# Performance work log

Hardware: AMD Instinct MI355X
Metric: run time of the kernel (lower is better)

The kernel has to match this reference:

```python
import jax, jax.numpy as jnp
import numpy as np

B, L, LM_DIM, D, R, NUM_LAYERS, C = 32, 1024, 1024, 128, 3, 2, 8
N = B * L
E = 524288
LN_EPS = 1e-5


def setup_inputs() -> dict:
    key = jax.random.key(0)
    ks = jax.random.split(key, 16)
    inp = {
        'output': jax.random.normal(ks[0], (B, L, LM_DIM), dtype=jnp.float32),
        'edge_index': jax.random.randint(ks[1], (2, E), 0, N, dtype=jnp.int64),
        'edge_type': jax.random.randint(ks[2], (E,), 0, R, dtype=jnp.int64),
        'attention_mask': jax.random.randint(ks[3], (B, L), 0, 2, dtype=jnp.int64),
        'labels': jax.random.randint(ks[4], (B, L), 0, C, dtype=jnp.int64),
        # parameters
        'lm_W': jax.random.normal(ks[5], (D, LM_DIM), dtype=jnp.float32) * 0.02,
        'lm_b': jnp.zeros((D,), dtype=jnp.float32),
        'ln_g': jnp.ones((D,), dtype=jnp.float32),
        'ln_b': jnp.zeros((D,), dtype=jnp.float32),
        'W_rel': jax.random.normal(ks[6], (NUM_LAYERS, R, D, D), dtype=jnp.float32) * 0.05,
        'W_root': jax.random.normal(ks[7], (NUM_LAYERS, D, D), dtype=jnp.float32) * 0.05,
        'conv_b': jnp.zeros((NUM_LAYERS, D), dtype=jnp.float32),
        'cls_W': jax.random.normal(ks[8], (C, 2 * D), dtype=jnp.float32) * 0.05,
        'cls_b': jnp.zeros((C,), dtype=jnp.float32),
    }
    return inp


def _forward(output, edge_index, edge_type, attention_mask, labels,
             lm_W, lm_b, ln_g, ln_b, W_rel, W_root, conv_b, cls_W, cls_b):
    # LM head + ReLU (dropout is identity in eval) + LayerNorm
    lm = jax.nn.relu(jnp.einsum('bld,hd->blh', output, lm_W) + lm_b)
    mu = jnp.mean(lm, axis=-1, keepdims=True)
    var = jnp.mean(jnp.square(lm - mu), axis=-1, keepdims=True)
    lm = (lm - mu) * jax.lax.rsqrt(var + LN_EPS) * ln_g + ln_b  # [B,L,D]

    # RGCN over flattened nodes
    x = lm.reshape(N, D)
    src, dst = edge_index[0], edge_index[1]
    seg = dst * R + edge_type  # combined (node, relation) segment id
    ones = jnp.ones((E,), dtype=x.dtype)
    cnt = jax.ops.segment_sum(ones, seg, num_segments=N * R).reshape(N, R, 1)
    denom = jnp.maximum(cnt, 1.0)
    for layer in range(NUM_LAYERS):
        x_src = x[src]  # [E,D] gather
        sums = jax.ops.segment_sum(x_src, seg, num_segments=N * R).reshape(N, R, D)
        mean_r = sums / denom  # per-relation mean aggregation (PyG RGCNConv aggr='mean')
        out = jnp.einsum('nrd,rde->ne', mean_r, W_rel[layer])
        out = out + x @ W_root[layer] + conv_b[layer]
        x = jax.nn.relu(out)  # dropout identity

    g = x.reshape(B, L, D)
    feat = jnp.concatenate([lm, g], axis=-1)  # [B,L,2D]
    logits = jnp.einsum('blh,ch->blc', feat, cls_W) + cls_b  # [B,L,C]

    # masked cross-entropy (ignore where attention_mask != 1)
    valid = (attention_mask.reshape(-1) == 1)
    logp = jax.nn.log_softmax(logits.reshape(-1, C), axis=-1)
    nll = -jnp.take_along_axis(logp, labels.reshape(-1, 1), axis=1)[:, 0]
    n_valid = jnp.maximum(jnp.sum(valid.astype(logits.dtype)), 1.0)
    loss = jnp.sum(jnp.where(valid, nll, 0.0)) / n_valid
    return loss, logits


def reference(output, edge_index, edge_type, attention_mask, labels,
              lm_W, lm_b, ln_g, ln_b, W_rel, W_root, conv_b, cls_W, cls_b):
    return _forward(output, edge_index, edge_type, attention_mask, labels,
                    lm_W, lm_b, ln_g, ln_b, W_rel, W_root, conv_b, cls_W, cls_b)
```

## Files before the change

### kernel.cpp

```cpp
#include <hip/hip_runtime.h>

#define Bb 32
#define Ll 1024
#define LMD 1024
#define Dd 128
#define Rr 3
#define NLAYER 2
#define Cc 8
#define Nn (Bb*Ll)
#define Ee 524288
#define NSEG (Nn*Rr)
#define LN_EPS 1e-5f

typedef __attribute__((ext_vector_type(8))) short bf16x8;
typedef __attribute__((ext_vector_type(4))) float f32x4;

__device__ inline short f2bf(float f) {
    unsigned u = __builtin_bit_cast(unsigned, f);
    u += 0x7fff + ((u >> 16) & 1);
    return (short)(u >> 16);
}
__device__ inline float bf2f(unsigned short s) {
    unsigned u = ((unsigned)s) << 16;
    return __builtin_bit_cast(float, u);
}

__global__ __launch_bounds__(256) void prep_kernel(
    const float* __restrict__ lmW, const float* __restrict__ Wrel,
    const float* __restrict__ Wroot, short* __restrict__ Wp_all,
    const int* __restrict__ dst, const int* __restrict__ et,
    int* __restrict__ counts)
{
    int bid = blockIdx.x;
    if (bid < 1024) {
        int idx = bid * 256 + threadIdx.x;
        float v;
        if (idx < 131072) {
            int kk = idx & 31, n = (idx >> 5) & 127, ks = idx >> 12;
            v = lmW[n * 1024 + ks * 32 + kk];
        } else {
            int j = idx - 131072;
            int layer = j >> 16;
            int kk = j & 31, n = (j >> 5) & 127, ks = (j >> 12) & 15;
            int k = ks * 32 + kk;
            v = (k < 384) ? Wrel[(size_t)layer * 49152 + (size_t)k * 128 + n]
                          : Wroot[(size_t)layer * 16384 + (size_t)(k - 384) * 128 + n];
        }
        Wp_all[idx] = f2bf(v);
    } else {
        int e = (bid - 1024) * 256 + threadIdx.x;
        atomicAdd(&counts[dst[e] * 3 + et[e]], 1);
    }
}

__global__ __launch_bounds__(256) void lm_gemm_ln_kernel(
    const float* __restrict__ A,
    const short* __restrict__ Wp,
    const float* __restrict__ bias,
    const float* __restrict__ lng, const float* __restrict__ lnb,
    short* __restrict__ lm_bf16)
{
    const int wv   = threadIdx.x >> 6;
    const int lane = threadIdx.x & 63;
    const int m16  = lane & 15;
    const int quad = lane >> 4;
    const int row_frag = blockIdx.x * 64 + wv * 16 + m16;
    const float* arow = A + (size_t)row_frag * 1024 + quad * 8;

    f32x4 acc[8];
    #pragma unroll
    for (int i = 0; i < 8; ++i) acc[i] = (f32x4){0.f, 0.f, 0.f, 0.f};

    #pragma unroll 2
    for (int ks = 0; ks < 32; ++ks) {
        const short* wpb = Wp + ks * 4096 + m16 * 32 + quad * 8;
        bf16x8 bfr[8];
        #pragma unroll
        for (int nt = 0; nt < 8; ++nt)
            bfr[nt] = *(const bf16x8*)(wpb + nt * 512);
        const float4* ap = (const float4*)(arow + ks * 32);
        float4 a0 = ap[0], a1 = ap[1];
        union { bf16x8 v; short s[8]; } af;
        af.s[0] = f2bf(a0.x); af.s[1] = f2bf(a0.y);
        af.s[2] = f2bf(a0.z); af.s[3] = f2bf(a0.w);
        af.s[4] = f2bf(a1.x); af.s[5] = f2bf(a1.y);
        af.s[6] = f2bf(a1.z); af.s[7] = f2bf(a1.w);
        #pragma unroll
        for (int nt = 0; nt < 8; ++nt)
            acc[nt] = __builtin_amdgcn_mfma_f32_16x16x32_bf16(af.v, bfr[nt], acc[nt], 0, 0, 0);
    }

    float v[8][4];
    #pragma unroll
    for (int nt = 0; nt < 8; ++nt) {
        float bs = bias[nt * 16 + m16];
        #pragma unroll
        for (int r = 0; r < 4; ++r) v[nt][r] = fmaxf(acc[nt][r] + bs, 0.f);
    }
    float gv[8], bv[8];
    #pragma unroll
    for (int nt = 0; nt < 8; ++nt) { gv[nt] = lng[nt * 16 + m16]; bv[nt] = lnb[nt * 16 + m16]; }

    const int row0 = blockIdx.x * 64 + wv * 16 + quad * 4;
    #pragma unroll
    for (int r = 0; r < 4; ++r) {
        float s = 0.f;
        #pragma unroll
        for (int nt = 0; nt < 8; ++nt) s += v[nt][r];
        s += __shfl_xor(s, 1, 64); s += __shfl_xor(s, 2, 64);
        s += __shfl_xor(s, 4, 64); s += __shfl_xor(s, 8, 64);
        float mu = s * (1.f / 128.f);
        float q = 0.f;
        #pragma unroll
        for (int nt = 0; nt < 8; ++nt) { float d = v[nt][r] - mu; q += d * d; }
        q += __shfl_xor(q, 1, 64); q += __shfl_xor(q, 2, 64);
        q += __shfl_xor(q, 4, 64); q += __shfl_xor(q, 8, 64);
        float rs = rsqrtf(q * (1.f / 128.f) + LN_EPS);
        size_t rowoff = (size_t)(row0 + r) * 128;
        #pragma unroll
        for (int nt = 0; nt < 8; ++nt) {
            float o = (v[nt][r] - mu) * rs * gv[nt] + bv[nt];
            lm_bf16[rowoff + nt * 16 + m16] = f2bf(o);
        }
    }
}

__global__ __launch_bounds__(256) void conv_gemm_kernel(
    const short* __restrict__ A1,
    const short* __restrict__ A2,
    const short* __restrict__ Wp,
    const float* __restrict__ bias,
    short* __restrict__ out_bf16)
{
    const int wv   = threadIdx.x >> 6;
    const int lane = threadIdx.x & 63;
    const int m16  = lane & 15;
    const int quad = lane >> 4;
    const int row_frag = blockIdx.x * 64 + wv * 16 + m16;
    const short* a1row = A1 + (size_t)row_frag * 384 + quad * 8;
    const short* a2row = A2 + (size_t)row_frag * 128 + quad * 8;

    f32x4 acc[8];
    #pragma unroll
    for (int i = 0; i < 8; ++i) acc[i] = (f32x4){0.f, 0.f, 0.f, 0.f};

    #pragma unroll 2
    for (int ks = 0; ks < 16; ++ks) {
        const short* wpb = Wp + ks * 4096 + m16 * 32 + quad * 8;
        bf16x8 bfr[8];
        #pragma unroll
        for (int nt = 0; nt < 8; ++nt)
            bfr[nt] = *(const bf16x8*)(wpb + nt * 512);
        const short* ar = (ks < 12) ? (a1row + ks * 32) : (a2row + (ks - 12) * 32);
        bf16x8 af = *(const bf16x8*)ar;
        #pragma unroll
        for (int nt = 0; nt < 8; ++nt)
            acc[nt] = __builtin_amdgcn_mfma_f32_16x16x32_bf16(af, bfr[nt], acc[nt], 0, 0, 0);
    }

    const int row0 = blockIdx.x * 64 + wv * 16 + quad * 4;
    #pragma unroll
    for (int nt = 0; nt < 8; ++nt) {
        float bs = bias[nt * 16 + m16];
        #pragma unroll
        for (int r = 0; r < 4; ++r) {
            float o = fmaxf(acc[nt][r] + bs, 0.f);
            out_bf16[(size_t)(row0 + r) * 128 + nt * 16 + m16] = f2bf(o);
        }
    }
}

__global__ __launch_bounds__(256) void scan_blk_kernel(
    const int* __restrict__ counts, int* __restrict__ excl, int* __restrict__ blksum)
{
    __shared__ int wsum[4];
    int t = threadIdx.x, lane = t & 63, wv = t >> 6;
    int g = blockIdx.x * 256 + t;
    int v = counts[g];
    int x = v;
    #pragma unroll
    for (int off = 1; off < 64; off <<= 1) {
        int y = __shfl_up(x, off, 64);
        if (lane >= off) x += y;
    }
    if (lane == 63) wsum[wv] = x;
    __syncthreads();
    int woff = 0;
    for (int i = 0; i < wv; ++i) woff += wsum[i];
    excl[g] = woff + x - v;
    if (t == 255) blksum[blockIdx.x] = woff + x;
}

__global__ __launch_bounds__(256) void scan_add_kernel(
    const int* __restrict__ excl, const int* __restrict__ blksum,
    int* __restrict__ row_ptr)
{
    __shared__ int ws4[4];
    __shared__ int off_sh;
    const int t = threadIdx.x, bid = blockIdx.x;
    int s = 0;
    for (int j = t; j < bid; j += 256) s += blksum[j];
    #pragma unroll
    for (int o = 32; o > 0; o >>= 1) s += __shfl_xor(s, o, 64);
    if ((t & 63) == 0) ws4[t >> 6] = s;
    __syncthreads();
    if (t == 0) off_sh = ws4[0] + ws4[1] + ws4[2] + ws4[3];
    __syncthreads();
    int g = bid * 256 + t;
    row_ptr[g] = excl[g] + off_sh;
    if (g == 0) row_ptr[NSEG] = Ee;
}

__global__ __launch_bounds__(256) void scatter_kernel(
    const int* __restrict__ src, const int* __restrict__ dst, const int* __restrict__ et,
    const int* __restrict__ row_ptr, int* __restrict__ fill, int* __restrict__ edge_src)
{
    int e = blockIdx.x * 256 + threadIdx.x;
    int s = dst[e] * 3 + et[e];
    int pos = row_ptr[s] + atomicAdd(&fill[s], 1);
    edge_src[pos] = src[e];
}

__global__ __launch_bounds__(256) void aggregate_kernel(
    const short* __restrict__ x, const int* __restrict__ row_ptr,
    const int* __restrict__ edge_src, short* __restrict__ agg)
{
    int seg  = blockIdx.x * 4 + (threadIdx.x >> 6);
    int lane = threadIdx.x & 63;
    int b = row_ptr[seg], e = row_ptr[seg + 1];
    int n = seg / 3, r = seg - n * 3;
    float ax = 0.f, ay = 0.f;
    int i = b;
    for (; i + 4 <= e; i += 4) {
        int s0 = edge_src[i],     s1 = edge_src[i + 1];
        int s2 = edge_src[i + 2], s3 = edge_src[i + 3];
        unsigned u0 = *(const unsigned*)(x + (size_t)s0 * 128 + lane * 2);
        unsigned u1 = *(const unsigned*)(x + (size_t)s1 * 128 + lane * 2);
        unsigned u2 = *(const unsigned*)(x + (size_t)s2 * 128 + lane * 2);
        unsigned u3 = *(const unsigned*)(x + (size_t)s3 * 128 + lane * 2);
        ax += bf2f((unsigned short)(u0 & 0xffff)) + bf2f((unsigned short)(u1 & 0xffff))
            + bf2f((unsigned short)(u2 & 0xffff)) + bf2f((unsigned short)(u3 & 0xffff));
        ay += bf2f((unsigned short)(u0 >> 16)) + bf2f((unsigned short)(u1 >> 16))
            + bf2f((unsigned short)(u2 >> 16)) + bf2f((unsigned short)(u3 >> 16));
    }
    for (; i + 2 <= e; i += 2) {
        int s0 = edge_src[i], s1 = edge_src[i + 1];
        unsigned u0 = *(const unsigned*)(x + (size_t)s0 * 128 + lane * 2);
        unsigned u1 = *(const unsigned*)(x + (size_t)s1 * 128 + lane * 2);
        ax += bf2f((unsigned short)(u0 & 0xffff)) + bf2f((unsigned short)(u1 & 0xffff));
        ay += bf2f((unsigned short)(u0 >> 16))    + bf2f((unsigned short)(u1 >> 16));
    }
    if (i < e) {
        int s0 = edge_src[i];
        unsigned u0 = *(const unsigned*)(x + (size_t)s0 * 128 + lane * 2);
        ax += bf2f((unsigned short)(u0 & 0xffff));
        ay += bf2f((unsigned short)(u0 >> 16));
    }
    int cnt = e - b;
    float inv = 1.f / (float)(cnt > 0 ? cnt : 1);
    unsigned short lo = (unsigned short)f2bf(ax * inv);
    unsigned short hi = (unsigned short)f2bf(ay * inv);
    *(unsigned*)(agg + (size_t)n * 384 + r * 128 + lane * 2) = (unsigned)lo | ((unsigned)hi << 16);
}

__global__ __launch_bounds__(256) void cls_loss_kernel(
    const short* __restrict__ lm, const short* __restrict__ g,
    const float* __restrict__ clsW, const float* __restrict__ clsb,
    const int* __restrict__ mask, const int* __restrict__ labels,
    float* __restrict__ logits, float* __restrict__ accb,
    unsigned* __restrict__ ticket, float* __restrict__ loss_out)
{
    __shared__ float W[2048];
    for (int i = threadIdx.x; i < 2048; i += 256) W[i] = clsW[i];
    __syncthreads();
    int n = blockIdx.x * 256 + threadIdx.x;
    float l[8];
    #pragma unroll
    for (int c = 0; c < 8; ++c) l[c] = clsb[c];
    const short* lmr = lm + (size_t)n * 128;
    const short* gr  = g  + (size_t)n * 128;
    #pragma unroll 2
    for (int h = 0; h < 128; h += 8) {
        uint4 raw = *(const uint4*)(lmr + h);
        float a[8];
        a[0] = bf2f((unsigned short)(raw.x & 0xffff)); a[1] = bf2f((unsigned short)(raw.x >> 16));
        a[2] = bf2f((unsigned short)(raw.y & 0xffff)); a[3] = bf2f((unsigned short)(raw.y >> 16));
        a[4] = bf2f((unsigned short)(raw.z & 0xffff)); a[5] = bf2f((unsigned short)(raw.z >> 16));
        a[6] = bf2f((unsigned short)(raw.w & 0xffff)); a[7] = bf2f((unsigned short)(raw.w >> 16));
        #pragma unroll
        for (int c = 0; c < 8; ++c) {
            const float* w = &W[c * 256 + h];
            #pragma unroll
            for (int j = 0; j < 8; ++j) l[c] = fmaf(a[j], w[j], l[c]);
        }
    }
    #pragma unroll 2
    for (int h = 0; h < 128; h += 8) {
        uint4 raw = *(const uint4*)(gr + h);
        float a[8];
        a[0] = bf2f((unsigned short)(raw.x & 0xffff)); a[1] = bf2f((unsigned short)(raw.x >> 16));
        a[2] = bf2f((unsigned short)(raw.y & 0xffff)); a[3] = bf2f((unsigned short)(raw.y >> 16));
        a[4] = bf2f((unsigned short)(raw.z & 0xffff)); a[5] = bf2f((unsigned short)(raw.z >> 16));
        a[6] = bf2f((unsigned short)(raw.w & 0xffff)); a[7] = bf2f((unsigned short)(raw.w >> 16));
        #pragma unroll
        for (int c = 0; c < 8; ++c) {
            const float* w = &W[c * 256 + 128 + h];
            #pragma unroll
            for (int j = 0; j < 8; ++j) l[c] = fmaf(a[j], w[j], l[c]);
        }
    }
    #pragma unroll
    for (int c = 0; c < 8; ++c) logits[(size_t)n * 8 + c] = l[c];

    float m = l[0];
    #pragma unroll
    for (int c = 1; c < 8; ++c) m = fmaxf(m, l[c]);
    float ss = 0.f;
    #pragma unroll
    for (int c = 0; c < 8; ++c) ss += expf(l[c] - m);
    float lse = m + logf(ss);
    int y = labels[n];
    float ly = l[0];
    #pragma unroll
    for (int c = 1; c < 8; ++c) ly = (y == c) ? l[c] : ly;
    float nll = lse - ly;
    bool valid = (mask[n] == 1);
    float lv = valid ? nll : 0.f;
    float cv = valid ? 1.f : 0.f;
    #pragma unroll
    for (int off = 32; off > 0; off >>= 1) {
        lv += __shfl_down(lv, off, 64);
        cv += __shfl_down(cv, off, 64);
    }
    if ((threadIdx.x & 63) == 0) { atomicAdd(&accb[0], lv); atomicAdd(&accb[1], cv); }

    __threadfence();
    if (threadIdx.x == 0) {
        unsigned t = atomicAdd(ticket, 1u);
        if (t == gridDim.x - 1) {
            float lsum = atomicAdd(&accb[0], 0.f);
            float csum = atomicAdd(&accb[1], 0.f);
            loss_out[0] = lsum / fmaxf(csum, 1.f);
        }
    }
}

extern "C" void kernel_launch(void* const* d_in, const int* in_sizes, int n_in,
                              void* d_out, int out_size, void* d_ws, size_t ws_size,
                              hipStream_t stream)
{
    const float* output = (const float*)d_in[0];
    const int* edge_index = (const int*)d_in[1];
    const int* edge_type  = (const int*)d_in[2];
    const int* attn       = (const int*)d_in[3];
    const int* labels     = (const int*)d_in[4];
    const float* lmW   = (const float*)d_in[5];
    const float* lmb   = (const float*)d_in[6];
    const float* lng   = (const float*)d_in[7];
    const float* lnb   = (const float*)d_in[8];
    const float* Wrel  = (const float*)d_in[9];
    const float* Wroot = (const float*)d_in[10];
    const float* convb = (const float*)d_in[11];
    const float* clsW  = (const float*)d_in[12];
    const float* clsb  = (const float*)d_in[13];

    char* ws = (char*)d_ws;
    short* lm_bf  = (short*)ws;                          ws += (size_t)Nn * Dd * 2;
    short* x1_bf  = (short*)ws;                          ws += (size_t)Nn * Dd * 2;
    short* x2_bf  = (short*)ws;                          ws += (size_t)Nn * Dd * 2;
    short* agg_bf = (short*)ws;                          ws += (size_t)Nn * 384 * 2;
    short* Wp_all = (short*)ws;                          ws += (size_t)262144 * 2;
    float* accb   = (float*)ws;                          ws += 64;
    int* counts   = (int*)ws;                            ws += (size_t)NSEG * 4;
    int* fill     = (int*)ws;                            ws += (size_t)NSEG * 4;
    int* row_ptr  = (int*)ws;                            ws += (size_t)(NSEG + 4) * 4;
    int* excl     = (int*)ws;                            ws += (size_t)NSEG * 4;
    int* blksum   = (int*)ws;                            ws += 512 * 4;
    int* edge_src = (int*)ws;

    unsigned* ticket = (unsigned*)(accb + 2);

    short* Wp_lm = Wp_all;
    short* Wp_c0 = Wp_all + 131072;
    short* Wp_c1 = Wp_all + 131072 + 65536;

    const int* e_src = edge_index;
    const int* e_dst = edge_index + Ee;

    hipMemsetAsync(accb, 0, 64 + 2 * (size_t)NSEG * 4, stream);

    prep_kernel<<<dim3(1024 + Ee / 256), dim3(256), 0, stream>>>(
        lmW, Wrel, Wroot, Wp_all, e_dst, edge_type, counts);

    lm_gemm_ln_kernel<<<dim3(Nn / 64), dim3(256), 0, stream>>>(
        output, Wp_lm, lmb, lng, lnb, lm_bf);

    scan_blk_kernel<<<dim3(NSEG / 256), dim3(256), 0, stream>>>(counts, excl, blksum);
    scan_add_kernel<<<dim3(NSEG / 256), dim3(256), 0, stream>>>(excl, blksum, row_ptr);
    scatter_kernel<<<dim3(Ee / 256), dim3(256), 0, stream>>>(
        e_src, e_dst, edge_type, row_ptr, fill, edge_src);

    aggregate_kernel<<<dim3(NSEG / 4), dim3(256), 0, stream>>>(lm_bf, row_ptr, edge_src, agg_bf);
    conv_gemm_kernel<<<dim3(Nn / 64), dim3(256), 0, stream>>>(
        agg_bf, lm_bf, Wp_c0, convb, x1_bf);
    aggregate_kernel<<<dim3(NSEG / 4), dim3(256), 0, stream>>>(x1_bf, row_ptr, edge_src, agg_bf);
    conv_gemm_kernel<<<dim3(Nn / 64), dim3(256), 0, stream>>>(
        agg_bf, x1_bf, Wp_c1, convb + Dd, x2_bf);

    float* logits = (float*)d_out + 1;
    cls_loss_kernel<<<dim3(Nn / 256), dim3(256), 0, stream>>>(
        lm_bf, x2_bf, clsW, clsb, attn, labels, logits, accb, ticket, (float*)d_out);
}
```

Baseline: 438.5 us.

## Fuse neighbor aggregation into conv GEMM via shared-memory staging

Replaces the separate aggregate and conv GEMM kernels with one kernel per layer that gathers and averages neighbor features for 64 nodes into LDS, then runs the MFMA GEMM reading the aggregated tile from LDS. This removes the global write and read of the aggregated buffer and two launches. In exchange, the gather now runs with far fewer waves (512 blocks of 4 waves, each serially handling many segments) and uses about 50KB of LDS per block, reducing latency hiding.

```diff
diff --git a/kernel.cpp b/kernel.cpp
--- a/kernel.cpp
+++ b/kernel.cpp
@@ -11,6 +11,7 @@
 #define Ee 524288
 #define NSEG (Nn*Rr)
 #define LN_EPS 1e-5f
+#define ASTRIDE 392
 
 typedef __attribute__((ext_vector_type(8))) short bf16x8;
 typedef __attribute__((ext_vector_type(4))) float f32x4;
@@ -125,20 +126,62 @@
     }
 }
 
-__global__ __launch_bounds__(256) void conv_gemm_kernel(
-    const short* __restrict__ A1,
-    const short* __restrict__ A2,
+__global__ __launch_bounds__(256) void agg_conv_kernel(
+    const short* __restrict__ x,
+    const int* __restrict__ row_ptr, const int* __restrict__ edge_src,
     const short* __restrict__ Wp,
     const float* __restrict__ bias,
     short* __restrict__ out_bf16)
 {
+    __shared__ short As[64 * ASTRIDE];
     const int wv   = threadIdx.x >> 6;
     const int lane = threadIdx.x & 63;
+    const int row0 = blockIdx.x * 64;
+
+    for (int si = wv; si < 192; si += 4) {
+        int i = si / 3, r = si - i * 3;
+        int seg = (row0 + i) * 3 + r;
+        int b = row_ptr[seg], e = row_ptr[seg + 1];
+        float ax = 0.f, ay = 0.f;
+        int j = b;
+        for (; j + 4 <= e; j += 4) {
+            int s0 = edge_src[j],     s1 = edge_src[j + 1];
+            int s2 = edge_src[j + 2], s3 = edge_src[j + 3];
+            unsigned u0 = *(const unsigned*)(x + (size_t)s0 * 128 + lane * 2);
+            unsigned u1 = *(const unsigned*)(x + (size_t)s1 * 128 + lane * 2);
+            unsigned u2 = *(const unsigned*)(x + (size_t)s2 * 128 + lane * 2);
+            unsigned u3 = *(const unsigned*)(x + (size_t)s3 * 128 + lane * 2);
+            ax += bf2f((unsigned short)(u0 & 0xffff)) + bf2f((unsigned short)(u1 & 0xffff))
+                + bf2f((unsigned short)(u2 & 0xffff)) + bf2f((unsigned short)(u3 & 0xffff));
+            ay += bf2f((unsigned short)(u0 >> 16)) + bf2f((unsigned short)(u1 >> 16))
+                + bf2f((unsigned short)(u2 >> 16)) + bf2f((unsigned short)(u3 >> 16));
+        }
+        for (; j + 2 <= e; j += 2) {
+            int s0 = edge_src[j], s1 = edge_src[j + 1];
+            unsigned u0 = *(const unsigned*)(x + (size_t)s0 * 128 + lane * 2);
+            unsigned u1 = *(const unsigned*)(x + (size_t)s1 * 128 + lane * 2);
+            ax += bf2f((unsigned short)(u0 & 0xffff)) + bf2f((unsigned short)(u1 & 0xffff));
+            ay += bf2f((unsigned short)(u0 >> 16))    + bf2f((unsigned short)(u1 >> 16));
+        }
+        if (j < e) {
+            int s0 = edge_src[j];
+            unsigned u0 = *(const unsigned*)(x + (size_t)s0 * 128 + lane * 2);
+            ax += bf2f((unsigned short)(u0 & 0xffff));
+            ay += bf2f((unsigned short)(u0 >> 16));
+        }
+        int cnt = e - b;
+        float inv = 1.f / (float)(cnt > 0 ? cnt : 1);
+        unsigned short lo = (unsigned short)f2bf(ax * inv);
+        unsigned short hi = (unsigned short)f2bf(ay * inv);
+        *(unsigned*)(&As[i * ASTRIDE + r * 128 + lane * 2]) =
+            (unsigned)lo | ((unsigned)hi << 16);
+    }
+    __syncthreads();
+
     const int m16  = lane & 15;
     const int quad = lane >> 4;
-    const int row_frag = blockIdx.x * 64 + wv * 16 + m16;
-    const short* a1row = A1 + (size_t)row_frag * 384 + quad * 8;
-    const short* a2row = A2 + (size_t)row_frag * 128 + quad * 8;
+    const int li   = wv * 16 + m16;
+    const short* a2row = x + (size_t)(row0 + li) * 128 + quad * 8;
 
     f32x4 acc[8];
     #pragma unroll
@@ -151,21 +194,22 @@
         #pragma unroll
         for (int nt = 0; nt < 8; ++nt)
             bfr[nt] = *(const bf16x8*)(wpb + nt * 512);
-        const short* ar = (ks < 12) ? (a1row + ks * 32) : (a2row + (ks - 12) * 32);
+        const short* ar = (ks < 12) ? (&As[li * ASTRIDE + ks * 32 + quad * 8])
+                                    : (a2row + (ks - 12) * 32);
         bf16x8 af = *(const bf16x8*)ar;
         #pragma unroll
         for (int nt = 0; nt < 8; ++nt)
             acc[nt] = __builtin_amdgcn_mfma_f32_16x16x32_bf16(af, bfr[nt], acc[nt], 0, 0, 0);
     }
 
-    const int row0 = blockIdx.x * 64 + wv * 16 + quad * 4;
+    const int orow0 = row0 + wv * 16 + quad * 4;
     #pragma unroll
     for (int nt = 0; nt < 8; ++nt) {
         float bs = bias[nt * 16 + m16];
         #pragma unroll
         for (int r = 0; r < 4; ++r) {
             float o = fmaxf(acc[nt][r] + bs, 0.f);
-            out_bf16[(size_t)(row0 + r) * 128 + nt * 16 + m16] = f2bf(o);
+            out_bf16[(size_t)(orow0 + r) * 128 + nt * 16 + m16] = f2bf(o);
         }
     }
 }
@@ -219,48 +263,6 @@
     int s = dst[e] * 3 + et[e];
     int pos = row_ptr[s] + atomicAdd(&fill[s], 1);
     edge_src[pos] = src[e];
-}
-
-__global__ __launch_bounds__(256) void aggregate_kernel(
-    const short* __restrict__ x, const int* __restrict__ row_ptr,
-    const int* __restrict__ edge_src, short* __restrict__ agg)
-{
-    int seg  = blockIdx.x * 4 + (threadIdx.x >> 6);
-    int lane = threadIdx.x & 63;
-    int b = row_ptr[seg], e = row_ptr[seg + 1];
-    int n = seg / 3, r = seg - n * 3;
-    float ax = 0.f, ay = 0.f;
-    int i = b;
-    for (; i + 4 <= e; i += 4) {
-        int s0 = edge_src[i],     s1 = edge_src[i + 1];
-        int s2 = edge_src[i + 2], s3 = edge_src[i + 3];
-        unsigned u0 = *(const unsigned*)(x + (size_t)s0 * 128 + lane * 2);
-        unsigned u1 = *(const unsigned*)(x + (size_t)s1 * 128 + lane * 2);
-        unsigned u2 = *(const unsigned*)(x + (size_t)s2 * 128 + lane * 2);
-        unsigned u3 = *(const unsigned*)(x + (size_t)s3 * 128 + lane * 2);
-        ax += bf2f((unsigned short)(u0 & 0xffff)) + bf2f((unsigned short)(u1 & 0xffff))
-            + bf2f((unsigned short)(u2 & 0xffff)) + bf2f((unsigned short)(u3 & 0xffff));
-        ay += bf2f((unsigned short)(u0 >> 16)) + bf2f((unsigned short)(u1 >> 16))
-            + bf2f((unsigned short)(u2 >> 16)) + bf2f((unsigned short)(u3 >> 16));
-    }
-    for (; i + 2 <= e; i += 2) {
-        int s0 = edge_src[i], s1 = edge_src[i + 1];
-        unsigned u0 = *(const unsigned*)(x + (size_t)s0 * 128 + lane * 2);
-        unsigned u1 = *(const unsigned*)(x + (size_t)s1 * 128 + lane * 2);
-        ax += bf2f((unsigned short)(u0 & 0xffff)) + bf2f((unsigned short)(u1 & 0xffff));
-        ay += bf2f((unsigned short)(u0 >> 16))    + bf2f((unsigned short)(u1 >> 16));
-    }
-    if (i < e) {
-        int s0 = edge_src[i];
-        unsigned u0 = *(const unsigned*)(x + (size_t)s0 * 128 + lane * 2);
-        ax += bf2f((unsigned short)(u0 & 0xffff));
-        ay += bf2f((unsigned short)(u0 >> 16));
-    }
-    int cnt = e - b;
-    float inv = 1.f / (float)(cnt > 0 ? cnt : 1);
-    unsigned short lo = (unsigned short)f2bf(ax * inv);
-    unsigned short hi = (unsigned short)f2bf(ay * inv);
-    *(unsigned*)(agg + (size_t)n * 384 + r * 128 + lane * 2) = (unsigned)lo | ((unsigned)hi << 16);
 }
 
 __global__ __launch_bounds__(256) void cls_loss_kernel(
@@ -368,7 +370,6 @@
     short* lm_bf  = (short*)ws;                          ws += (size_t)Nn * Dd * 2;
     short* x1_bf  = (short*)ws;                          ws += (size_t)Nn * Dd * 2;
     short* x2_bf  = (short*)ws;                          ws += (size_t)Nn * Dd * 2;
-    short* agg_bf = (short*)ws;                          ws += (size_t)Nn * 384 * 2;
     short* Wp_all = (short*)ws;                          ws += (size_t)262144 * 2;
     float* accb   = (float*)ws;                          ws += 64;
     int* counts   = (int*)ws;                            ws += (size_t)NSEG * 4;
@@ -400,12 +401,10 @@
     scatter_kernel<<<dim3(Ee / 256), dim3(256), 0, stream>>>(
         e_src, e_dst, edge_type, row_ptr, fill, edge_src);
 
-    aggregate_kernel<<<dim3(NSEG / 4), dim3(256), 0, stream>>>(lm_bf, row_ptr, edge_src, agg_bf);
-    conv_gemm_kernel<<<dim3(Nn / 64), dim3(256), 0, stream>>>(
-        agg_bf, lm_bf, Wp_c0, convb, x1_bf);
-    aggregate_kernel<<<dim3(NSEG / 4), dim3(256), 0, stream>>>(x1_bf, row_ptr, edge_src, agg_bf);
-    conv_gemm_kernel<<<dim3(Nn / 64), dim3(256), 0, stream>>>(
-        agg_bf, x1_bf, Wp_c1, convb + Dd, x2_bf);
+    agg_conv_kernel<<<dim3(Nn / 64), dim3(256), 0, stream>>>(
+        lm_bf, row_ptr, edge_src, Wp_c0, convb, x1_bf);
+    agg_conv_kernel<<<dim3(Nn / 64), dim3(256), 0, stream>>>(
+        x1_bf, row_ptr, edge_src, Wp_c1, convb + Dd, x2_bf);
 
     float* logits = (float*)d_out + 1;
     cls_loss_kernel<<<dim3(Nn / 256), dim3(256), 0, stream>>>(
```

Result: slower. 510.8 us (+16.5%).
